# Kernel tuning notes

Hardware: AMD Instinct MI355X
Metric: run time of the kernel (lower is better)

The kernel has to match this reference:

```python
import jax, jax.numpy as jnp
import numpy as np

DIM = 1024
HEADS = 16
HIDDEN = 4096
EPS = 1e-5


def layernorm(x, w, b):
    mu = jnp.mean(x, axis=-1, keepdims=True)
    var = jnp.var(x, axis=-1, keepdims=True)
    return (x - mu) * jax.lax.rsqrt(var + EPS) * w + b


def setup_inputs() -> dict:
    key = jax.random.key(0)
    ks = jax.random.split(key, 12)
    s = lambda fan_in: 1.0 / np.sqrt(fan_in)
    return {
        "x": jax.random.normal(ks[0], (8, 1024, DIM), dtype=jnp.float32),
        "norm1_w": jnp.ones((DIM,), jnp.float32),
        "norm1_b": jnp.zeros((DIM,), jnp.float32),
        "qkv_w": jax.random.uniform(ks[1], (3 * DIM, DIM), jnp.float32, -s(DIM), s(DIM)),
        "proj_w": jax.random.uniform(ks[2], (DIM, DIM), jnp.float32, -s(DIM), s(DIM)),
        "proj_b": jax.random.uniform(ks[3], (DIM,), jnp.float32, -s(DIM), s(DIM)),
        "norm2_w": jnp.ones((DIM,), jnp.float32),
        "norm2_b": jnp.zeros((DIM,), jnp.float32),
        "fc1_w": jax.random.uniform(ks[4], (HIDDEN, DIM), jnp.float32, -s(DIM), s(DIM)),
        "fc1_b": jax.random.uniform(ks[5], (HIDDEN,), jnp.float32, -s(DIM), s(DIM)),
        "fc2_w": jax.random.uniform(ks[6], (DIM, HIDDEN), jnp.float32, -s(HIDDEN), s(HIDDEN)),
        "fc2_b": jax.random.uniform(ks[7], (DIM,), jnp.float32, -s(HIDDEN), s(HIDDEN)),
    }


def reference(x, norm1_w, norm1_b, qkv_w, proj_w, proj_b,
              norm2_w, norm2_b, fc1_w, fc1_b, fc2_w, fc2_b):
    B, N, C = x.shape
    hd = C // HEADS
    scale = hd ** -0.5

    # ---- attention branch ----
    xn = layernorm(x, norm1_w, norm1_b)
    qkv_tmp = jnp.einsum('bnc,oc->bno', xn, qkv_w)          # [B,N,3C]
    qkv = qkv_tmp.reshape(B, N, 3, HEADS, hd).transpose(2, 0, 3, 1, 4)
    q, k, v = qkv[0], qkv[1], qkv[2]                         # [B,H,N,hd]
    qkv_out = qkv_tmp.reshape(B, N, 3, C).transpose(2, 0, 1, 3)
    attn = jnp.einsum('bhnd,bhmd->bhnm', q, k) * scale       # [B,H,N,N]
    attn = jax.nn.softmax(attn, axis=-1)
    ao = jnp.einsum('bhnm,bhmd->bhnd', attn, v)              # [B,H,N,hd]
    ao = ao.transpose(0, 2, 1, 3).reshape(B, N, C)
    attn_out = jnp.einsum('bnc,oc->bno', ao, proj_w) + proj_b
    x = x + attn_out

    # ---- mlp branch ----
    xn2 = layernorm(x, norm2_w, norm2_b)
    h = jnp.einsum('bnc,hc->bnh', xn2, fc1_w) + fc1_b
    h = jax.nn.gelu(h, approximate=False)
    hidden_out = jnp.einsum('bnh,ch->bnc', h, fc2_w) + fc2_b
    x = x + hidden_out
    return (x, (qkv_out[0], qkv_out[1], qkv_out[2]), hidden_out)
```

## Files before the change

### kernel.cpp

```cpp
#include <hip/hip_runtime.h>
#include <hip/hip_bf16.h>

typedef __attribute__((ext_vector_type(8))) __bf16 bf16x8;
typedef __attribute__((ext_vector_type(4))) float f32x4;
typedef unsigned short u16;
typedef unsigned int u32;

#define TOK 8192
#define C_DIM 1024
#define OUT_SEC 8388608

__device__ __forceinline__ u16 f2bf(float f) {
  return __builtin_bit_cast(u16, __float2bfloat16(f));
}

__device__ __forceinline__ int cvt_pk_bf16(float lo, float hi) {
  int r;
  asm("v_cvt_pk_bf16_f32 %0, %1, %2" : "=v"(r) : "v"(lo), "v"(hi));
  return r;
}

__device__ __forceinline__ float max3f(float a, float b, float c) {
  return fmaxf(fmaxf(a, b), c);
}

__device__ __forceinline__ void gl_lds16(const void* g, void* l) {
  __builtin_amdgcn_global_load_lds(
      (__attribute__((address_space(1))) void*)const_cast<void*>(g),
      (__attribute__((address_space(3))) void*)l, 16, 0, 0);
}

__device__ __forceinline__ float gelu_f(float x) {
  float y = 0.7978845608f * (x + 0.044715f * x * x * x);
  y = fminf(fmaxf(y, -15.f), 15.f);
  float e = __expf(2.0f * y);
  float th = (e - 1.0f) / (e + 1.0f);
  return 0.5f * x * (1.0f + th);
}

__global__ __launch_bounds__(256) void cvt_kernel(const float* __restrict__ in,
                                                  u16* __restrict__ out, int n4) {
  int i = blockIdx.x * blockDim.x + threadIdx.x;
  if (i >= n4) return;
  float4 v = reinterpret_cast<const float4*>(in)[i];
  alignas(8) u16 pk[4];
  pk[0] = f2bf(v.x); pk[1] = f2bf(v.y); pk[2] = f2bf(v.z); pk[3] = f2bf(v.w);
  reinterpret_cast<uint2*>(out)[i] = *reinterpret_cast<uint2*>(pk);
}

__global__ __launch_bounds__(256) void ln_kernel(const float* __restrict__ x,
                                                 const float* __restrict__ w,
                                                 const float* __restrict__ b,
                                                 u16* __restrict__ out) {
  const int row = blockIdx.x;
  const int t = threadIdx.x;
  const float* xr = x + (size_t)row * C_DIM;
  float4 v = reinterpret_cast<const float4*>(xr)[t];
  float s = v.x + v.y + v.z + v.w;
  float ss = v.x * v.x + v.y * v.y + v.z * v.z + v.w * v.w;
#pragma unroll
  for (int off = 1; off < 64; off <<= 1) {
    s += __shfl_xor(s, off, 64);
    ss += __shfl_xor(ss, off, 64);
  }
  __shared__ float red[8];
  const int wv = t >> 6;
  if ((t & 63) == 0) { red[wv] = s; red[4 + wv] = ss; }
  __syncthreads();
  s = red[0] + red[1] + red[2] + red[3];
  ss = red[4] + red[5] + red[6] + red[7];
  const float mu = s * (1.0f / C_DIM);
  const float var = ss * (1.0f / C_DIM) - mu * mu;
  const float rstd = rsqrtf(var + 1e-5f);
  float4 w4 = reinterpret_cast<const float4*>(w)[t];
  float4 b4 = reinterpret_cast<const float4*>(b)[t];
  alignas(8) u16 pk[4];
  pk[0] = f2bf((v.x - mu) * rstd * w4.x + b4.x);
  pk[1] = f2bf((v.y - mu) * rstd * w4.y + b4.y);
  pk[2] = f2bf((v.z - mu) * rstd * w4.z + b4.z);
  pk[3] = f2bf((v.w - mu) * rstd * w4.w + b4.w);
  reinterpret_cast<uint2*>(out + (size_t)row * C_DIM)[t] = *reinterpret_cast<uint2*>(pk);
}

__global__ __launch_bounds__(256) void vtrans_kernel(const float* __restrict__ vsrc,
                                                     u16* __restrict__ vt) {
  const int bh = blockIdx.x, nt = blockIdx.y;
  const int b = bh >> 4, h = bh & 15;
  const int t = threadIdx.x;
  __shared__ u16 T[64][65];
#pragma unroll
  for (int p = 0; p < 4; ++p) {
    const int idx = p * 256 + t;
    const int n = idx >> 4, d4 = (idx & 15) * 4;
    float4 x4 = *reinterpret_cast<const float4*>(
        vsrc + (size_t)(b * 1024 + nt * 64 + n) * 1024 + h * 64 + d4);
    T[d4 + 0][n] = f2bf(x4.x);
    T[d4 + 1][n] = f2bf(x4.y);
    T[d4 + 2][n] = f2bf(x4.z);
    T[d4 + 3][n] = f2bf(x4.w);
  }
  __syncthreads();
  const int d = t >> 2, ns = (t & 3) * 16;
  u16* dst = vt + (size_t)bh * 65536 + (size_t)d * 1024 + nt * 64 + ns;
  alignas(16) u16 tmp[16];
#pragma unroll
  for (int i = 0; i < 16; ++i) tmp[i] = T[d][ns + i];
  reinterpret_cast<uint4*>(dst)[0] = reinterpret_cast<uint4*>(tmp)[0];
  reinterpret_cast<uint4*>(dst)[1] = reinterpret_cast<uint4*>(tmp)[1];
}

#define MFMA_T(AF, BF, BASE)                                                \
  _Pragma("unroll") for (int nf = 0; nf < 4; ++nf) {                        \
    _Pragma("unroll") for (int mf = 0; mf < 4; ++mf)                        \
        acc[(BASE) + mf][nf] = __builtin_amdgcn_mfma_f32_16x16x32_bf16(     \
            AF[mf], BF[nf], acc[(BASE) + mf][nf], 0, 0, 0);                 \
  }

enum { EPI8_FC1 = 0 };

template <int EPI>
__global__ __launch_bounds__(512, 2) void gemm8(
    const u16* __restrict__ A, const u16* __restrict__ Bw,
    const float* __restrict__ bias,
    float* __restrict__ out, u16* __restrict__ h1, u16* __restrict__ h2,
    int K) {
  extern __shared__ char smem[];
  const int t = threadIdx.x, lane = t & 63, wid = t >> 6;
  const int wm = wid >> 2, wn = wid & 3;

  const int k8 = blockIdx.x & 7, jj = blockIdx.x >> 3;
  const int brow0 = (k8 * 4 + (jj & 3)) * 256;
  const int bcol0 = (jj >> 2) * 256;

  const int NT = K >> 6;

  f32x4 zero = {0.f, 0.f, 0.f, 0.f};
  f32x4 acc[8][4];
#pragma unroll
  for (int m = 0; m < 8; ++m)
#pragma unroll
    for (int n = 0; n < 4; ++n) acc[m][n] = zero;

  const int src_slot = ((t & 3) ^ ((t >> 3) & 3)) * 8;
  const int srow = t >> 2;
  auto stage = [&](int buf, int mat, int ks, int ktile) {
    const u16* G = mat ? Bw : A;
    const int gr0 = mat ? bcol0 : brow0;
    const int k0 = ktile * 64 + ks * 32 + src_slot;
    char* dst = smem + ((buf << 16) | (mat << 15) | (ks << 14));
#pragma unroll
    for (int i = 0; i < 2; ++i)
      gl_lds16(G + (size_t)(gr0 + i * 128 + srow) * K + k0, dst + i * 8192 + t * 16);
  };

  const int swz16 = (((lane >> 4) ^ ((lane >> 1) & 3)) << 4);
  const int l15 = lane & 15;

  stage(0, 0, 0, 0);
  stage(0, 1, 0, 0);
  stage(0, 0, 1, 0);
  stage(0, 1, 1, 0);
  asm volatile("s_waitcnt vmcnt(4)" ::: "memory");
  __builtin_amdgcn_s_barrier();

  for (int tt = 0; tt < NT; ++tt) {
    char* As_ = smem + ((tt & 1) << 16);
    char* Bs_ = As_ + 32768;
    const int nbuf = (tt & 1) ^ 1;
    const bool pf = (tt + 1 < NT);
    bf16x8 af[4], af2[4], bfr[4];

    auto LDA = [&](bf16x8* dst8, int MH, int KK) {
#pragma unroll
      for (int mf = 0; mf < 4; ++mf)
        dst8[mf] = *reinterpret_cast<const bf16x8*>(
            As_ + KK * 16384 + (wm * 128 + MH * 64 + mf * 16 + l15) * 64 + swz16);
    };
    auto LDB = [&](int KK) {
#pragma unroll
      for (int nf = 0; nf < 4; ++nf)
        bfr[nf] = *reinterpret_cast<const bf16x8*>(
            Bs_ + KK * 16384 + (wn * 64 + nf * 16 + l15) * 64 + swz16);
    };

    LDB(0);
    LDA(af, 0, 0);
    __builtin_amdgcn_sched_barrier(0);
    LDA(af2, 1, 0);
    __builtin_amdgcn_sched_barrier(0);
    if (pf) { stage(nbuf, 0, 0, tt + 1); stage(nbuf, 1, 0, tt + 1); }
    asm volatile("s_waitcnt lgkmcnt(4)" ::: "memory");
    __builtin_amdgcn_sched_barrier(0);
    __builtin_amdgcn_s_setprio(1);
    MFMA_T(af, bfr, 0)
    asm volatile("s_waitcnt lgkmcnt(0)" ::: "memory");
    __builtin_amdgcn_sched_barrier(0);
    MFMA_T(af2, bfr, 4)
    __builtin_amdgcn_s_setprio(0);
    if (pf) {
      asm volatile("s_waitcnt vmcnt(4)" ::: "memory");
    } else {
      asm volatile("s_waitcnt vmcnt(0)" ::: "memory");
    }
    __builtin_amdgcn_s_barrier();

    LDB(1);
    LDA(af, 1, 1);
    __builtin_amdgcn_sched_barrier(0);
    LDA(af2, 0, 1);
    __builtin_amdgcn_sched_barrier(0);
    if (pf) { stage(nbuf, 0, 1, tt + 1); stage(nbuf, 1, 1, tt + 1); }
    asm volatile("s_waitcnt lgkmcnt(4)" ::: "memory");
    __builtin_amdgcn_sched_barrier(0);
    __builtin_amdgcn_s_setprio(1);
    MFMA_T(af, bfr, 4)
    asm volatile("s_waitcnt lgkmcnt(0)" ::: "memory");
    __builtin_amdgcn_sched_barrier(0);
    MFMA_T(af2, bfr, 0)
    __builtin_amdgcn_s_setprio(0);
    if (pf)
      asm volatile("s_waitcnt vmcnt(4)" ::: "memory");
    __builtin_amdgcn_s_barrier();
  }

  const int rb = brow0 + wm * 128;
  const int cb = bcol0 + wn * 64;
#pragma unroll
  for (int m = 0; m < 8; ++m) {
#pragma unroll
    for (int n = 0; n < 4; ++n) {
      const int c = cb + n * 16 + l15;
#pragma unroll
      for (int j = 0; j < 4; ++j) {
        const int r = rb + m * 16 + (lane >> 4) * 4 + j;
        float v = acc[m][n][j];
        v += bias[c];
        h1[(size_t)r * 4096 + c] = f2bf(gelu_f(v));
      }
    }
  }
}

enum { EPIN_PROJ = 0, EPIN_FC2 = 1, EPIN_QKV = 2 };

template <int EPI>
__global__ __launch_bounds__(512, 1) void gemm8n(
    const u16* __restrict__ A, const u16* __restrict__ Bw,
    const float* __restrict__ bias, const float* resid,
    float* out, float* out2_f, u16* __restrict__ h1, u16* __restrict__ h2,
    int K) {
  extern __shared__ char smem[];
  const int t = threadIdx.x, lane = t & 63, wid = t >> 6;
  const int wm = wid >> 2, wn = wid & 3;

  const int k8 = blockIdx.x & 7, jj = blockIdx.x >> 3;
  const int brow0 = (k8 * 8 + (jj & 7)) * 128;
  const int bcol0 = (jj >> 3) * 256;

  const int NT = K >> 6;

  f32x4 zero = {0.f, 0.f, 0.f, 0.f};
  f32x4 acc[4][4];
#pragma unroll
  for (int m = 0; m < 4; ++m)
#pragma unroll
    for (int n = 0; n < 4; ++n) acc[m][n] = zero;

  const int src_slot = ((t & 3) ^ ((t >> 3) & 3)) * 8;
  const int srow = t >> 2;
  auto stage_all = [&](char* dst, int ktile) {
#pragma unroll
    for (int ks = 0; ks < 2; ++ks) {
      const int k0 = ktile * 64 + ks * 32 + src_slot;
      gl_lds16(A + (size_t)(brow0 + srow) * K + k0, dst + ks * 8192 + t * 16);
    }
#pragma unroll
    for (int ks = 0; ks < 2; ++ks) {
      const int k0 = ktile * 64 + ks * 32 + src_slot;
      char* db = dst + 16384 + ks * 16384;
#pragma unroll
      for (int i = 0; i < 2; ++i)
        gl_lds16(Bw + (size_t)(bcol0 + i * 128 + srow) * K + k0, db + i * 8192 + t * 16);
    }
  };

  const int swz16 = (((lane >> 4) ^ ((lane >> 1) & 3)) << 4);
  const int l15 = lane & 15;

  char* bcur = smem;
  char* bnxt = smem + 49152;
  char* bspr = smem + 98304;

  stage_all(bcur, 0);
  stage_all(bnxt, 1);
  asm volatile("s_waitcnt vmcnt(6)" ::: "memory");
  __builtin_amdgcn_s_barrier();

  for (int tt = 0; tt < NT; ++tt) {
    const bool pf2 = (tt + 2 < NT);
    bf16x8 af[4], af2[4], bfr[4], bfr2[4];

    auto LDA = [&](bf16x8* dst8, int KK) {
#pragma unroll
      for (int mf = 0; mf < 4; ++mf)
        dst8[mf] = *reinterpret_cast<const bf16x8*>(
            bcur + KK * 8192 + (wm * 64 + mf * 16 + l15) * 64 + swz16);
    };
    auto LDB = [&](bf16x8* dst8, int KK) {
#pragma unroll
      for (int nf = 0; nf < 4; ++nf)
        dst8[nf] = *reinterpret_cast<const bf16x8*>(
            bcur + 16384 + KK * 16384 + (wn * 64 + nf * 16 + l15) * 64 + swz16);
    };

    LDA(af, 0);
    LDB(bfr, 0);
    __builtin_amdgcn_sched_barrier(0);
    LDA(af2, 1);
    LDB(bfr2, 1);
    __builtin_amdgcn_sched_barrier(0);
    if (pf2) stage_all(bspr, tt + 2);
    asm volatile("s_waitcnt lgkmcnt(8)" ::: "memory");
    __builtin_amdgcn_sched_barrier(0);
    __builtin_amdgcn_s_setprio(1);
    MFMA_T(af, bfr, 0)
    asm volatile("s_waitcnt lgkmcnt(0)" ::: "memory");
    __builtin_amdgcn_sched_barrier(0);
    MFMA_T(af2, bfr2, 0)
    __builtin_amdgcn_s_setprio(0);
    if (pf2) {
      asm volatile("s_waitcnt vmcnt(6)" ::: "memory");
    } else {
      asm volatile("s_waitcnt vmcnt(0)" ::: "memory");
    }
    __builtin_amdgcn_s_barrier();

    char* tmp = bcur;
    bcur = bnxt;
    bnxt = bspr;
    bspr = tmp;
  }

  const int rb = brow0 + wm * 64;
  const int cb = bcol0 + wn * 64;
#pragma unroll
  for (int m = 0; m < 4; ++m) {
#pragma unroll
    for (int n = 0; n < 4; ++n) {
      const int c = cb + n * 16 + l15;
#pragma unroll
      for (int j = 0; j < 4; ++j) {
        const int r = rb + m * 16 + (lane >> 4) * 4 + j;
        float v = acc[m][n][j];
        if constexpr (EPI == EPIN_PROJ) {
          v += bias[c] + resid[(size_t)r * 1024 + c];
          out[(size_t)r * 1024 + c] = v;
        } else if constexpr (EPI == EPIN_FC2) {
          v += bias[c];
          out[(size_t)r * 1024 + c] = v;
          out2_f[(size_t)r * 1024 + c] = resid[(size_t)r * 1024 + c] + v;
        } else {
          const int sec = c >> 10, cc = c & 1023;
          out[(size_t)sec * OUT_SEC + (size_t)r * 1024 + cc] = v;
          const size_t boff =
              (((size_t)(r >> 10) * 16 + (cc >> 6)) * 1024 + (r & 1023)) * 64 + (cc & 63);
          if (sec == 0) h1[boff] = f2bf(v * 0.18033688f);
          else if (sec == 1) h2[boff] = f2bf(v);
        }
      }
    }
  }
}

__global__ __launch_bounds__(256, 4) void attn_kernel(const u16* __restrict__ Qb,
                                                      const u16* __restrict__ Kb,
                                                      const u16* __restrict__ Vtb,
                                                      u16* __restrict__ ao) {
  const int orig = blockIdx.y * gridDim.x + blockIdx.x;
  const int wid = (orig & 7) * 128 + (orig >> 3);
  const int bh = wid >> 3;
  const int qt = wid & 7;
  const int b = bh >> 4, h = bh & 15;
  const int t = threadIdx.x, lane = t & 63, wv = t >> 6;
  const int l15 = lane & 15, g = lane >> 4;

  __shared__ u16 KV[2][8192];

  const int q0 = qt * 128 + wv * 32;
  bf16x8 qfA[2], qfB[2];
#pragma unroll
  for (int c = 0; c < 2; ++c) {
    qfA[c] = *reinterpret_cast<const bf16x8*>(
        Qb + (size_t)bh * 65536 + (size_t)(q0 + l15) * 64 + c * 32 + g * 8);
    qfB[c] = *reinterpret_cast<const bf16x8*>(
        Qb + (size_t)bh * 65536 + (size_t)(q0 + 16 + l15) * 64 + c * 32 + g * 8);
  }

  f32x4 zero = {0.f, 0.f, 0.f, 0.f};
  f32x4 accO0[4], accO1[4];
#pragma unroll
  for (int nb = 0; nb < 4; ++nb) { accO0[nb] = zero; accO1[nb] = zero; }
  float m0 = -1e30f, m1 = -1e30f, lr0 = 0.f, lr1 = 0.f;

  const char* ktile0 = (const char*)(Kb + (size_t)bh * 65536);
  const char* vbase = (const char*)(Vtb + (size_t)bh * 65536);

  auto stage = [&](int buf, int kv0) {
    char* base = (char*)KV[buf];
#pragma unroll
    for (int i = 0; i < 2; ++i) {
      const int o = i * 4096 + t * 16;
      const int row = o >> 7, colb = o & 127;
      const int swz = colb ^ ((row & 7) << 4);
      gl_lds16(ktile0 + (size_t)kv0 * 128 + (size_t)row * 128 + swz, base + o);
      gl_lds16(vbase + (size_t)row * 2048 + (size_t)kv0 * 2 + swz, base + 8192 + o);
    }
  };

  stage(0, 0);
  int cur = 0;

  const int a0 = (l15 + ((g & 1) << 5)) << 2;
  const int a1 = a0 + 64;
  const bool up = (lane & 32) != 0;

  for (int tile = 0; tile < 16; ++tile) {
    asm volatile("s_waitcnt vmcnt(0)" ::: "memory");
    __builtin_amdgcn_s_barrier();
    if (tile + 1 < 16) stage(cur ^ 1, (tile + 1) * 64);

    const char* kcur = (const char*)KV[cur];
    const char* vcur = kcur + 8192;

    f32x4 s0[4], s1[4];
#pragma unroll
    for (int jb = 0; jb < 4; ++jb) { s0[jb] = zero; s1[jb] = zero; }
#pragma unroll
    for (int jb = 0; jb < 4; ++jb)
#pragma unroll
      for (int c = 0; c < 2; ++c) {
        const int row = jb * 16 + l15;
        const int colb = c * 64 + g * 16;
        bf16x8 kf = *reinterpret_cast<const bf16x8*>(
            kcur + row * 128 + (colb ^ ((row & 7) << 4)));
        s0[jb] = __builtin_amdgcn_mfma_f32_16x16x32_bf16(kf, qfA[c], s0[jb], 0, 0, 0);
        s1[jb] = __builtin_amdgcn_mfma_f32_16x16x32_bf16(kf, qfB[c], s1[jb], 0, 0, 0);
      }

    int w0[4][2], w1[4][2];
    {
      float ta = max3f(s0[0][0], s0[0][1], s0[0][2]);
      float tb = max3f(s0[0][3], s0[1][0], s0[1][1]);
      float tc = max3f(s0[1][2], s0[1][3], s0[2][0]);
      float td = max3f(s0[2][1], s0[2][2], s0[2][3]);
      float te = max3f(s0[3][0], s0[3][1], s0[3][2]);
      float mt = max3f(max3f(ta, tb, tc), max3f(td, te, s0[3][3]), -1e30f);
      mt = fmaxf(mt, __shfl_xor(mt, 16, 64));
      mt = fmaxf(mt, __shfl_xor(mt, 32, 64));
      if (!__all(mt <= m0 + 8.0f)) {
        const float mn = fmaxf(m0, mt);
        const float sc = exp2f(m0 - mn);
        lr0 *= sc;
#pragma unroll
        for (int nb = 0; nb < 4; ++nb) accO0[nb] *= sc;
        m0 = mn;
      }
      float rs = 0.f;
#pragma unroll
      for (int jb = 0; jb < 4; ++jb)
#pragma unroll
        for (int r = 0; r < 4; ++r) {
          const float p = exp2f(s0[jb][r] - m0);
          s0[jb][r] = p;
          rs += p;
        }
      lr0 += rs;
#pragma unroll
      for (int jb = 0; jb < 4; ++jb) {
        w0[jb][0] = cvt_pk_bf16(s0[jb][0], s0[jb][1]);
        w0[jb][1] = cvt_pk_bf16(s0[jb][2], s0[jb][3]);
      }
    }
    {
      float ta = max3f(s1[0][0], s1[0][1], s1[0][2]);
      float tb = max3f(s1[0][3], s1[1][0], s1[1][1]);
      float tc = max3f(s1[1][2], s1[1][3], s1[2][0]);
      float td = max3f(s1[2][1], s1[2][2], s1[2][3]);
      float te = max3f(s1[3][0], s1[3][1], s1[3][2]);
      float mt = max3f(max3f(ta, tb, tc), max3f(td, te, s1[3][3]), -1e30f);
      mt = fmaxf(mt, __shfl_xor(mt, 16, 64));
      mt = fmaxf(mt, __shfl_xor(mt, 32, 64));
      if (!__all(mt <= m1 + 8.0f)) {
        const float mn = fmaxf(m1, mt);
        const float sc = exp2f(m1 - mn);
        lr1 *= sc;
#pragma unroll
        for (int nb = 0; nb < 4; ++nb) accO1[nb] *= sc;
        m1 = mn;
      }
      float rs = 0.f;
#pragma unroll
      for (int jb = 0; jb < 4; ++jb)
#pragma unroll
        for (int r = 0; r < 4; ++r) {
          const float p = exp2f(s1[jb][r] - m1);
          s1[jb][r] = p;
          rs += p;
        }
      lr1 += rs;
#pragma unroll
      for (int jb = 0; jb < 4; ++jb) {
        w1[jb][0] = cvt_pk_bf16(s1[jb][0], s1[jb][1]);
        w1[jb][1] = cvt_pk_bf16(s1[jb][2], s1[jb][3]);
      }
    }

#pragma unroll
    for (int c = 0; c < 2; ++c) {
      int p0w0 = __builtin_amdgcn_ds_bpermute(a0, w0[2 * c][0]);
      int p0w0h = __builtin_amdgcn_ds_bpermute(a0, w0[2 * c + 1][0]);
      int p0w1 = __builtin_amdgcn_ds_bpermute(a0, w0[2 * c][1]);
      int p0w1h = __builtin_amdgcn_ds_bpermute(a0, w0[2 * c + 1][1]);
      int p0w2 = __builtin_amdgcn_ds_bpermute(a1, w0[2 * c][0]);
      int p0w2h = __builtin_amdgcn_ds_bpermute(a1, w0[2 * c + 1][0]);
      int p0w3 = __builtin_amdgcn_ds_bpermute(a1, w0[2 * c][1]);
      int p0w3h = __builtin_amdgcn_ds_bpermute(a1, w0[2 * c + 1][1]);
      alignas(16) int word0[4] = {up ? p0w0h : p0w0, up ? p0w1h : p0w1,
                                  up ? p0w2h : p0w2, up ? p0w3h : p0w3};
      bf16x8 pf0 = *reinterpret_cast<bf16x8*>(word0);

      int p1w0 = __builtin_amdgcn_ds_bpermute(a0, w1[2 * c][0]);
      int p1w0h = __builtin_amdgcn_ds_bpermute(a0, w1[2 * c + 1][0]);
      int p1w1 = __builtin_amdgcn_ds_bpermute(a0, w1[2 * c][1]);
      int p1w1h = __builtin_amdgcn_ds_bpermute(a0, w1[2 * c + 1][1]);
      int p1w2 = __builtin_amdgcn_ds_bpermute(a1, w1[2 * c][0]);
      int p1w2h = __builtin_amdgcn_ds_bpermute(a1, w1[2 * c + 1][0]);
      int p1w3 = __builtin_amdgcn_ds_bpermute(a1, w1[2 * c][1]);
      int p1w3h = __builtin_amdgcn_ds_bpermute(a1, w1[2 * c + 1][1]);
      alignas(16) int word1[4] = {up ? p1w0h : p1w0, up ? p1w1h : p1w1,
                                  up ? p1w2h : p1w2, up ? p1w3h : p1w3};
      bf16x8 pf1 = *reinterpret_cast<bf16x8*>(word1);

#pragma unroll
      for (int nb = 0; nb < 4; ++nb) {
        const int row = nb * 16 + l15;
        const int colb = c * 64 + g * 16;
        bf16x8 vf = *reinterpret_cast<const bf16x8*>(
            vcur + row * 128 + (colb ^ ((row & 7) << 4)));
        accO0[nb] = __builtin_amdgcn_mfma_f32_16x16x32_bf16(vf, pf0, accO0[nb], 0, 0, 0);
        accO1[nb] = __builtin_amdgcn_mfma_f32_16x16x32_bf16(vf, pf1, accO1[nb], 0, 0, 0);
      }
    }

    cur ^= 1;
  }

  lr0 += __shfl_xor(lr0, 16, 64);
  lr0 += __shfl_xor(lr0, 32, 64);
  lr1 += __shfl_xor(lr1, 16, 64);
  lr1 += __shfl_xor(lr1, 32, 64);
  const float rl0 = __builtin_amdgcn_rcpf(lr0);
  const float rl1 = __builtin_amdgcn_rcpf(lr1);

  u16* dst0 = ao + (size_t)(b * 1024 + q0 + l15) * 1024 + h * 64 + g * 4;
  u16* dst1 = ao + (size_t)(b * 1024 + q0 + 16 + l15) * 1024 + h * 64 + g * 4;
#pragma unroll
  for (int nb = 0; nb < 4; ++nb) {
    alignas(8) u16 pk0[4], pk1[4];
#pragma unroll
    for (int j = 0; j < 4; ++j) {
      pk0[j] = f2bf(accO0[nb][j] * rl0);
      pk1[j] = f2bf(accO1[nb][j] * rl1);
    }
    *reinterpret_cast<uint2*>(dst0 + nb * 16) = *reinterpret_cast<uint2*>(pk0);
    *reinterpret_cast<uint2*>(dst1 + nb * 16) = *reinterpret_cast<uint2*>(pk1);
  }
}

extern "C" void kernel_launch(void* const* d_in, const int* in_sizes, int n_in,
                              void* d_out, int out_size, void* d_ws, size_t ws_size,
                              hipStream_t stream) {
  const float* x      = (const float*)d_in[0];
  const float* n1w    = (const float*)d_in[1];
  const float* n1b    = (const float*)d_in[2];
  const float* qkv_w  = (const float*)d_in[3];
  const float* proj_w = (const float*)d_in[4];
  const float* proj_b = (const float*)d_in[5];
  const float* n2w    = (const float*)d_in[6];
  const float* n2b    = (const float*)d_in[7];
  const float* fc1_w  = (const float*)d_in[8];
  const float* fc1_b  = (const float*)d_in[9];
  const float* fc2_w  = (const float*)d_in[10];
  const float* fc2_b  = (const float*)d_in[11];
  float* out = (float*)d_out;

  u16* wsb    = (u16*)d_ws;
  u16* w_qkv  = wsb;
  u16* w_proj = wsb + 3145728;
  u16* w_fc1  = wsb + 4194304;
  u16* w_fc2  = wsb + 8388608;
  u16* xn     = wsb + 12582912;
  u16* Qb     = wsb + 20971520;
  u16* Kb     = wsb + 29360128;
  u16* Vtw    = wsb + 37748736;
  u16* ao     = wsb + 46137344;
  u16* hbuf   = wsb + 20971520;

  (void)hipFuncSetAttribute((const void*)gemm8<EPI8_FC1>,
                            hipFuncAttributeMaxDynamicSharedMemorySize, 131072);
  (void)hipFuncSetAttribute((const void*)gemm8n<EPIN_PROJ>,
                            hipFuncAttributeMaxDynamicSharedMemorySize, 147456);
  (void)hipFuncSetAttribute((const void*)gemm8n<EPIN_FC2>,
                            hipFuncAttributeMaxDynamicSharedMemorySize, 147456);
  (void)hipFuncSetAttribute((const void*)gemm8n<EPIN_QKV>,
                            hipFuncAttributeMaxDynamicSharedMemorySize, 147456);

  cvt_kernel<<<3072, 256, 0, stream>>>(qkv_w, w_qkv, 786432);
  cvt_kernel<<<1024, 256, 0, stream>>>(proj_w, w_proj, 262144);
  cvt_kernel<<<4096, 256, 0, stream>>>(fc1_w, w_fc1, 1048576);
  cvt_kernel<<<4096, 256, 0, stream>>>(fc2_w, w_fc2, 1048576);

  ln_kernel<<<TOK, 256, 0, stream>>>(x, n1w, n1b, xn);
  gemm8n<EPIN_QKV><<<768, 512, 147456, stream>>>(
      xn, w_qkv, nullptr, nullptr, out + OUT_SEC, nullptr, Qb, Kb, 1024);
  vtrans_kernel<<<dim3(128, 16), 256, 0, stream>>>(out + 3 * (size_t)OUT_SEC, Vtw);
  attn_kernel<<<dim3(128, 8), 256, 0, stream>>>(Qb, Kb, Vtw, ao);
  gemm8n<EPIN_PROJ><<<256, 512, 147456, stream>>>(
      ao, w_proj, proj_b, x, out, nullptr, nullptr, nullptr, 1024);
  ln_kernel<<<TOK, 256, 0, stream>>>(out, n2w, n2b, xn);
  gemm8<EPI8_FC1><<<512, 512, 131072, stream>>>(
      xn, w_fc1, fc1_b, nullptr, hbuf, nullptr, 1024);
  gemm8n<EPIN_FC2><<<256, 512, 147456, stream>>>(
      hbuf, w_fc2, fc2_b, out, out + 4 * (size_t)OUT_SEC, out, nullptr, nullptr, 4096);
}
```

Before: 385.8 us.

## Shrink FC1 GEMM K-tile to 32 with simpler double-buffered pipeline

Restructures the FC1 GEMM main loop to use a K-tile of 32 instead of 64, so each double buffer holds one 32-wide slice of A and B. This cuts dynamic LDS from 128 KB to 64 KB and replaces the split two-half schedule with a single wait-barrier-prefetch-compute step per iteration. The goal is lower LDS use, which could allow more resident blocks, and a simpler schedule. In exchange there are twice as many barriers and full vmcnt(0) waits per K, which may expose global-load latency.

```diff
diff --git a/kernel.cpp b/kernel.cpp
--- a/kernel.cpp
+++ b/kernel.cpp
@@ -132,7 +132,7 @@
   const int brow0 = (k8 * 4 + (jj & 3)) * 256;
   const int bcol0 = (jj >> 2) * 256;
 
-  const int NT = K >> 6;
+  const int NT = K >> 5;
 
   f32x4 zero = {0.f, 0.f, 0.f, 0.f};
   f32x4 acc[8][4];
@@ -143,52 +143,45 @@
 
   const int src_slot = ((t & 3) ^ ((t >> 3) & 3)) * 8;
   const int srow = t >> 2;
-  auto stage = [&](int buf, int mat, int ks, int ktile) {
-    const u16* G = mat ? Bw : A;
-    const int gr0 = mat ? bcol0 : brow0;
-    const int k0 = ktile * 64 + ks * 32 + src_slot;
-    char* dst = smem + ((buf << 16) | (mat << 15) | (ks << 14));
+  auto stage = [&](int buf, int ktile) {
+    const int k0 = ktile * 32 + src_slot;
+    char* dst = smem + (buf << 15);
 #pragma unroll
     for (int i = 0; i < 2; ++i)
-      gl_lds16(G + (size_t)(gr0 + i * 128 + srow) * K + k0, dst + i * 8192 + t * 16);
+      gl_lds16(A + (size_t)(brow0 + i * 128 + srow) * K + k0, dst + i * 8192 + t * 16);
+#pragma unroll
+    for (int i = 0; i < 2; ++i)
+      gl_lds16(Bw + (size_t)(bcol0 + i * 128 + srow) * K + k0,
+               dst + 16384 + i * 8192 + t * 16);
   };
 
   const int swz16 = (((lane >> 4) ^ ((lane >> 1) & 3)) << 4);
   const int l15 = lane & 15;
 
-  stage(0, 0, 0, 0);
-  stage(0, 1, 0, 0);
-  stage(0, 0, 1, 0);
-  stage(0, 1, 1, 0);
-  asm volatile("s_waitcnt vmcnt(4)" ::: "memory");
-  __builtin_amdgcn_s_barrier();
+  stage(0, 0);
 
   for (int tt = 0; tt < NT; ++tt) {
-    char* As_ = smem + ((tt & 1) << 16);
-    char* Bs_ = As_ + 32768;
-    const int nbuf = (tt & 1) ^ 1;
-    const bool pf = (tt + 1 < NT);
+    char* cur = smem + ((tt & 1) << 15);
     bf16x8 af[4], af2[4], bfr[4];
 
-    auto LDA = [&](bf16x8* dst8, int MH, int KK) {
-#pragma unroll
-      for (int mf = 0; mf < 4; ++mf)
-        dst8[mf] = *reinterpret_cast<const bf16x8*>(
-            As_ + KK * 16384 + (wm * 128 + MH * 64 + mf * 16 + l15) * 64 + swz16);
-    };
-    auto LDB = [&](int KK) {
-#pragma unroll
-      for (int nf = 0; nf < 4; ++nf)
-        bfr[nf] = *reinterpret_cast<const bf16x8*>(
-            Bs_ + KK * 16384 + (wn * 64 + nf * 16 + l15) * 64 + swz16);
-    };
-
-    LDB(0);
-    LDA(af, 0, 0);
-    __builtin_amdgcn_sched_barrier(0);
-    LDA(af2, 1, 0);
-    __builtin_amdgcn_sched_barrier(0);
-    if (pf) { stage(nbuf, 0, 0, tt + 1); stage(nbuf, 1, 0, tt + 1); }
+    asm volatile("s_waitcnt vmcnt(0)" ::: "memory");
+    __builtin_amdgcn_s_barrier();
+    if (tt + 1 < NT) stage((tt & 1) ^ 1, tt + 1);
+
+#pragma unroll
+    for (int nf = 0; nf < 4; ++nf)
+      bfr[nf] = *reinterpret_cast<const bf16x8*>(
+          cur + 16384 + (wn * 64 + nf * 16 + l15) * 64 + swz16);
+#pragma unroll
+    for (int mf = 0; mf < 4; ++mf)
+      af[mf] = *reinterpret_cast<const bf16x8*>(
+          cur + (wm * 128 + mf * 16 + l15) * 64 + swz16);
+    __builtin_amdgcn_sched_barrier(0);
+#pragma unroll
+    for (int mf = 0; mf < 4; ++mf)
+      af2[mf] = *reinterpret_cast<const bf16x8*>(
+          cur + (wm * 128 + 64 + mf * 16 + l15) * 64 + swz16);
+    __builtin_amdgcn_sched_barrier(0);
     asm volatile("s_waitcnt lgkmcnt(4)" ::: "memory");
     __builtin_amdgcn_sched_barrier(0);
     __builtin_amdgcn_s_setprio(1);
@@ -197,30 +190,6 @@
     __builtin_amdgcn_sched_barrier(0);
     MFMA_T(af2, bfr, 4)
     __builtin_amdgcn_s_setprio(0);
-    if (pf) {
-      asm volatile("s_waitcnt vmcnt(4)" ::: "memory");
-    } else {
-      asm volatile("s_waitcnt vmcnt(0)" ::: "memory");
-    }
-    __builtin_amdgcn_s_barrier();
-
-    LDB(1);
-    LDA(af, 1, 1);
-    __builtin_amdgcn_sched_barrier(0);
-    LDA(af2, 0, 1);
-    __builtin_amdgcn_sched_barrier(0);
-    if (pf) { stage(nbuf, 0, 1, tt + 1); stage(nbuf, 1, 1, tt + 1); }
-    asm volatile("s_waitcnt lgkmcnt(4)" ::: "memory");
-    __builtin_amdgcn_sched_barrier(0);
-    __builtin_amdgcn_s_setprio(1);
-    MFMA_T(af, bfr, 4)
-    asm volatile("s_waitcnt lgkmcnt(0)" ::: "memory");
-    __builtin_amdgcn_sched_barrier(0);
-    MFMA_T(af2, bfr, 0)
-    __builtin_amdgcn_s_setprio(0);
-    if (pf)
-      asm volatile("s_waitcnt vmcnt(4)" ::: "memory");
-    __builtin_amdgcn_s_barrier();
   }
 
   const int rb = brow0 + wm * 128;
@@ -607,7 +576,7 @@
   u16* hbuf   = wsb + 20971520;
 
   (void)hipFuncSetAttribute((const void*)gemm8<EPI8_FC1>,
-                            hipFuncAttributeMaxDynamicSharedMemorySize, 131072);
+                            hipFuncAttributeMaxDynamicSharedMemorySize, 65536);
   (void)hipFuncSetAttribute((const void*)gemm8n<EPIN_PROJ>,
                             hipFuncAttributeMaxDynamicSharedMemorySize, 147456);
   (void)hipFuncSetAttribute((const void*)gemm8n<EPIN_FC2>,
@@ -628,7 +597,7 @@
   gemm8n<EPIN_PROJ><<<256, 512, 147456, stream>>>(
       ao, w_proj, proj_b, x, out, nullptr, nullptr, nullptr, 1024);
   ln_kernel<<<TOK, 256, 0, stream>>>(out, n2w, n2b, xn);
-  gemm8<EPI8_FC1><<<512, 512, 131072, stream>>>(
+  gemm8<EPI8_FC1><<<512, 512, 65536, stream>>>(
       xn, w_fc1, fc1_b, nullptr, hbuf, nullptr, 1024);
   gemm8n<EPIN_FC2><<<256, 512, 147456, stream>>>(
       hbuf, w_fc2, fc2_b, out, out + 4 * (size_t)OUT_SEC, out, nullptr, nullptr, 4096);
```

Measured after the change: 392.6 us. No clear change (+1.7%).
